# Kernel tuning notes

Measured on AMD Instinct MI355X. Metric: run time of the kernel, lower is better.

The kernel has to match this reference:

```python
import jax, jax.numpy as jnp
import numpy as np
import math

Q_DIM = 1024
K_DIM = 1024
ATT_DIM = 1024
POS_DIM = 64
B, NQ, NK = 4, 2048, 2048
EPS = 1e-5


def _ln(x, g, b):
    m = jnp.mean(x, axis=-1, keepdims=True)
    v = jnp.var(x, axis=-1, keepdims=True)
    return (x - m) * jax.lax.rsqrt(v + EPS) * g + b


def _sinpos(n, dim):
    # SinPos: exp = 2*arange(dim//2)/dim; pos = p * 10000**-exp; cat(pos, pos+pi/2); sin
    e = 2.0 * jnp.arange(dim // 2, dtype=jnp.float32) / dim      # [dim/2]
    p = jnp.arange(n, dtype=jnp.float32)[:, None]                # [n,1]
    ph = p * jnp.power(10000.0, -e)[None, :]                     # [n,dim/2]
    return jnp.sin(jnp.concatenate([ph, ph + math.pi / 2], axis=1))  # [n,dim]


def setup_inputs() -> dict:
    key = jax.random.key(0)
    ks = jax.random.split(key, 8)
    s = 0.02
    return {
        "q": jax.random.normal(ks[0], (B, NQ, Q_DIM), jnp.float32),
        "k": jax.random.normal(ks[1], (B, NK, K_DIM), jnp.float32),
        "Wq": jax.random.normal(ks[2], (Q_DIM, ATT_DIM), jnp.float32) * s,
        "bq": jnp.zeros((ATT_DIM,), jnp.float32),
        "Wk": jax.random.normal(ks[3], (K_DIM, ATT_DIM), jnp.float32) * s,
        "bk": jnp.zeros((ATT_DIM,), jnp.float32),
        "Wv": jax.random.normal(ks[4], (K_DIM, ATT_DIM), jnp.float32) * s,
        "bv": jnp.zeros((ATT_DIM,), jnp.float32),
        "gq": jnp.ones((ATT_DIM,), jnp.float32), "betaq": jnp.zeros((ATT_DIM,), jnp.float32),
        "gk": jnp.ones((ATT_DIM,), jnp.float32), "betak": jnp.zeros((ATT_DIM,), jnp.float32),
        "gv": jnp.ones((ATT_DIM,), jnp.float32), "betav": jnp.zeros((ATT_DIM,), jnp.float32),
        "Wp": jax.random.normal(ks[5], (POS_DIM, POS_DIM), jnp.float32) * s,
        "bp": jnp.zeros((POS_DIM,), jnp.float32),
    }


def reference(q, k, Wq, bq, Wk, bk, Wv, bv, gq, betaq, gk, betak, gv, betav, Wp, bp):
    qn = _ln(q @ Wq + bq, gq, betaq)          # [B,NQ,D]
    vn = _ln(k @ Wv + bv, gv, betav)          # [B,NK,D]
    kn = _ln(k @ Wk + bk, gk, betak)          # [B,NK,D]
    pos = _sinpos(NK, POS_DIM)                # [NK,P]

    # attention 1: Q=qn, K=kn, V=pos
    s1 = jnp.einsum('bnd,bjd->bnj', qn, kn) * (1.0 / math.sqrt(ATT_DIM))
    a1 = jax.nn.softmax(s1, axis=-1)          # [B,NQ,NK]
    x = jnp.einsum('bnj,jp->bnp', a1, pos)    # [B,NQ,P]

    # pos_net (Linear)
    x = x @ Wp + bp                           # [B,NQ,P]

    # attention 2: Q=x, K=pos, V=vn
    s2 = jnp.einsum('bnp,jp->bnj', x, pos) * (1.0 / math.sqrt(POS_DIM))
    a2 = jax.nn.softmax(s2, axis=-1)          # [B,NQ,NK]
    out = jnp.einsum('bnj,bjd->bnd', a2, vn)  # [B,NQ,D]

    att = jnp.stack([a1, a2], axis=1)         # [B,2,NQ,NK] == torch.cat over head dim
    return out, att
```

## Files before the change

### kernel.cpp

```cpp
#include <hip/hip_runtime.h>
#include <math.h>
#include <stdint.h>


typedef _Float16 f16;
typedef _Float16 f16x4 __attribute__((ext_vector_type(4)));
typedef _Float16 f16x8 __attribute__((ext_vector_type(8)));
typedef float f32x4 __attribute__((ext_vector_type(4)));

static constexpr int CB  = 4;
static constexpr int CNQ = 2048;
static constexpr int CNK = 2048;
static constexpr int CD  = 1024;
static constexpr int CP  = 64;

static __device__ __forceinline__ void async16(const f16* gp, f16* lp) {
  __builtin_amdgcn_global_load_lds(
      (const __attribute__((address_space(1))) void*)(uintptr_t)gp,
      (__attribute__((address_space(3))) void*)(uint32_t)(uintptr_t)lp,
      16, 0, 0);
}

__global__ __launch_bounds__(256) void prep_kernel(
    const float* __restrict__ q, const float* __restrict__ k,
    const float* __restrict__ Wq, const float* __restrict__ Wk,
    const float* __restrict__ Wv,
    f16* __restrict__ q16, f16* __restrict__ k16,
    f16* __restrict__ WqT, f16* __restrict__ WkvT,
    f16* __restrict__ posb, f16* __restrict__ posTb) {
  const int b = blockIdx.x;
  if (b < 512) {
    int tid = b * 256 + threadIdx.x;
    int p = tid >> 11;
    int j = tid & (CNK - 1);
    int i = p & 31;
    float ph = (float)j * powf(10000.0f, -(float)i * (1.0f / 32.0f));
    float v = (p < 32) ? sinf(ph) : cosf(ph);
    posb[j * CP + p]   = (f16)v;
    posTb[p * CNK + j] = (f16)v;
  } else if (b < 512 + 16384) {
    const int NF4 = CB * CNQ * CD / 4;
    int tid = (b - 512) * 256 + threadIdx.x;
    const float* src = (tid < NF4) ? q : k;
    f16* dst = (tid < NF4) ? q16 : k16;
    int i = (tid < NF4) ? tid : tid - NF4;
    float4 v = reinterpret_cast<const float4*>(src)[i];
    f16x4 o = {(f16)v.x, (f16)v.y, (f16)v.z, (f16)v.w};
    reinterpret_cast<f16x4*>(dst)[i] = o;
  } else {
    __shared__ float t[64][65];
    const int idx = b - 16896;
    const int z = idx >> 8;
    const int rem = idx & 255;
    const float* W = (z == 0) ? Wq : (z == 1) ? Wk : Wv;
    f16* WT = (z == 0) ? WqT : (z == 1) ? WkvT : WkvT + 1024 * 1024;
    int k0 = (rem & 15) * 64, n0 = (rem >> 4) * 64;
    int tx = threadIdx.x & 63, ty = threadIdx.x >> 6;
#pragma unroll
    for (int i = 0; i < 16; i++)
      t[ty + 4 * i][tx] = W[(size_t)(k0 + ty + 4 * i) * CD + n0 + tx];
    __syncthreads();
#pragma unroll
    for (int i = 0; i < 16; i++)
      WT[(size_t)(n0 + 4 * i + ty) * CD + k0 + tx] = (f16)t[tx][ty + 4 * i];
  }
}

template <int BM, int BN>
__device__ __forceinline__ void gemm_core2(
    const f16* __restrict__ Ab, const f16* __restrict__ Bb,
    int lda, int ldb, int K, int m0, int n0, f16* sm,
    f32x4 (&acc)[BM / 32][4]) {
  constexpr int FM = BM / 32;
  constexpr int TI = (BM + BN) / 64;
  constexpr int bufsz = (BM + BN) * 64;
  const int tid = threadIdx.x;
  const int lane = tid & 63, wid = tid >> 6;
  const int wr = wid >> 2, wc = wid & 3;
  const int lrow = lane & 15, kg = lane >> 4;

  auto stage = [&](int i, int kt, int buf) {
    const int s = i * 512 + tid;
    const int row = s >> 3;
    const int cb = (s & 7) << 4;
    const int scb = cb ^ ((row & 7) << 4);
    const f16* src = (i < BM / 64)
        ? Ab + (size_t)(m0 + row) * lda + kt * 64 + (scb >> 1)
        : Bb + (size_t)(n0 + row - BM) * ldb + kt * 64 + (scb >> 1);
    async16(src, &sm[buf * bufsz + s * 8]);
  };

  const int NTk = K >> 6;
#pragma unroll
  for (int i = 0; i < TI; i++) stage(i, 0, 0);

  for (int t = 0; t < NTk; ++t) {
    const int cur = t & 1;
    if (t + 1 < NTk) {
#pragma unroll
      for (int i = 0; i < TI; i++) stage(i, t + 1, cur ^ 1);
      if constexpr (TI == 8) asm volatile("s_waitcnt vmcnt(8)" ::: "memory");
      else                   asm volatile("s_waitcnt vmcnt(6)" ::: "memory");
    } else {
      asm volatile("s_waitcnt vmcnt(0)" ::: "memory");
    }
    __builtin_amdgcn_s_barrier();

    const f16* smA = sm + cur * bufsz;
    const f16* smB = smA + BM * 64;
    __builtin_amdgcn_s_setprio(1);
#pragma unroll
    for (int kk = 0; kk < 2; ++kk) {
      const int Cb = kk * 64 + kg * 16;
      f16x8 af[FM], bf[4];
#pragma unroll
      for (int m = 0; m < FM; ++m) {
        const int ar = wr * (BM / 2) + m * 16 + lrow;
        af[m] = *reinterpret_cast<const f16x8*>(
            &smA[ar * 64 + ((Cb ^ ((ar & 7) << 4)) >> 1)]);
      }
#pragma unroll
      for (int n = 0; n < 4; ++n) {
        const int br = wc * 64 + n * 16 + lrow;
        bf[n] = *reinterpret_cast<const f16x8*>(
            &smB[br * 64 + ((Cb ^ ((br & 7) << 4)) >> 1)]);
      }
#pragma unroll
      for (int m = 0; m < FM; ++m)
#pragma unroll
        for (int n = 0; n < 4; ++n)
          acc[m][n] = __builtin_amdgcn_mfma_f32_16x16x32_f16(af[m], bf[n], acc[m][n], 0, 0, 0);
    }
    __builtin_amdgcn_s_setprio(0);
    __builtin_amdgcn_s_barrier();
  }
}

template <int BM, int BN>
__device__ __forceinline__ void epi_f16(
    f32x4 (&acc)[BM / 32][4], f16* sm, f16* Cp, int ldc, int m0, int n0) {
  const int tid = threadIdx.x, lane = tid & 63, wid = tid >> 6;
  const int wr = wid >> 2, wc = wid & 3;
  const int rbase = wr * (BM / 2) + (lane >> 4) * 4;
  const int cbase = wc * 64 + (lane & 15);
  __syncthreads();
#pragma unroll
  for (int mg = 0; mg < BM / 32; mg++)
#pragma unroll
    for (int n = 0; n < 4; n++)
#pragma unroll
      for (int r = 0; r < 4; r++)
        sm[(rbase + mg * 16 + r) * BN + cbase + n * 16] = (f16)acc[mg][n][r];
  __syncthreads();
  constexpr int CH = BM * BN / (512 * 8);
#pragma unroll
  for (int c = 0; c < CH; c++) {
    const int idx = c * 512 + tid;
    const int row = idx / (BN / 8);
    const int cole = (idx % (BN / 8)) * 8;
    f16x8 v = *reinterpret_cast<const f16x8*>(&sm[row * BN + cole]);
    *reinterpret_cast<f16x8*>(Cp + (size_t)(m0 + row) * ldc + n0 + cole) = v;
  }
}

template <int BM, int BN>
__device__ __forceinline__ void epi_exp(
    f32x4 (&acc)[BM / 32][4], f16* sm, float* psum, f16* Cp, int ldc,
    int m0, int n0, float scale, float* PSrow) {
  constexpr int SL = BN / 8;
  const int tid = threadIdx.x, lane = tid & 63, wid = tid >> 6;
  const int wr = wid >> 2, wc = wid & 3;
  const int rbase = wr * (BM / 2) + (lane >> 4) * 4;
  const int cbase = wc * 64 + (lane & 15);
  __syncthreads();
#pragma unroll
  for (int mg = 0; mg < BM / 32; mg++)
#pragma unroll
    for (int n = 0; n < 4; n++)
#pragma unroll
      for (int r = 0; r < 4; r++)
        sm[(rbase + mg * 16 + r) * BN + cbase + n * 16] =
            (f16)__expf(acc[mg][n][r] * scale);
  __syncthreads();
  constexpr int CH = BM * BN / (512 * 8);
#pragma unroll
  for (int c = 0; c < CH; c++) {
    const int idx = c * 512 + tid;
    const int row = idx / SL;
    const int cole = (idx % SL) * 8;
    f16x8 v = *reinterpret_cast<const f16x8*>(&sm[row * BN + cole]);
    *reinterpret_cast<f16x8*>(Cp + (size_t)(m0 + row) * ldc + n0 + cole) = v;
    float p = 0.f;
#pragma unroll
    for (int j = 0; j < 8; j++) p += (float)v[j];
#pragma unroll
    for (int o = 1; o < SL; o <<= 1) p += __shfl_xor(p, o);
    if ((lane & (SL - 1)) == 0) psum[row] = p;
  }
  __syncthreads();
  if (tid < BM) PSrow[tid] = psum[tid];
}

template <int BM, int BN>
__device__ __forceinline__ void epi_f32(
    f32x4 (&acc)[BM / 32][4], f16* smh, float* Cp, int ldc, int m0, int n0) {
  float* st = (float*)smh;
  const int tid = threadIdx.x, lane = tid & 63, wid = tid >> 6;
  const int wr = wid >> 2, wc = wid & 3;
  const int cbase = wc * 64 + (lane & 15);
#pragma unroll
  for (int half = 0; half < 2; half++) {
    __syncthreads();
    if (wr == half) {
#pragma unroll
      for (int mg = 0; mg < BM / 32; mg++)
#pragma unroll
        for (int r = 0; r < 4; r++) {
          const int rloc = (lane >> 4) * 4 + mg * 16 + r;
#pragma unroll
          for (int n = 0; n < 4; n++)
            st[rloc * BN + cbase + n * 16] = acc[mg][n][r];
        }
    }
    __syncthreads();
    constexpr int CH = (BM / 2) * BN / (512 * 4);
#pragma unroll
    for (int c = 0; c < CH; c++) {
      const int idx = c * 512 + tid;
      const int row = idx / (BN / 4);
      const int cole = (idx % (BN / 4)) * 4;
      f32x4 v = *reinterpret_cast<const f32x4*>(&st[row * BN + cole]);
      *reinterpret_cast<f32x4*>(
          Cp + (size_t)(m0 + half * (BM / 2) + row) * ldc + n0 + cole) = v;
    }
  }
}

__global__ __launch_bounds__(512) void gemmIn_kernel(
    const f16* __restrict__ q16, const f16* __restrict__ WqT, f16* __restrict__ tmpq,
    const f16* __restrict__ k16, const f16* __restrict__ WkvT, f16* __restrict__ tmp2) {
  __shared__ __attribute__((aligned(16))) f16 sm[2 * (128 + 256) * 64];
  const int b = blockIdx.x;
  const int swz = (b & 7) * 96 + (b >> 3);
  const f16 *A, *B;
  f16* C;
  int ldc, m0, n0;
  if (swz < 256) {
    const int bx = swz & 63, by = swz >> 6;
    A = q16; B = WqT; C = tmpq; ldc = 1024; m0 = bx * 128; n0 = by * 256;
  } else {
    const int idx = swz - 256;
    const int bx = idx & 63, by = idx >> 6;
    A = k16; B = WkvT; C = tmp2; ldc = 2048; m0 = bx * 128; n0 = by * 256;
  }
  f32x4 acc[4][4] = {};
  gemm_core2<128, 256>(A, B, 1024, 1024, 1024, m0, n0, sm, acc);
  epi_f16<128, 256>(acc, sm, C, ldc, m0, n0);
}

__global__ __launch_bounds__(512) void gemmS1_kernel(
    const f16* __restrict__ qn, const f16* __restrict__ kn,
    f16* __restrict__ e1, float* __restrict__ PS) {
  __shared__ __attribute__((aligned(16))) f16 sm[2 * (256 + 256) * 64];
  __shared__ float psum[256];
  const int b = blockIdx.x;
  const int swz = (b & 7) * 32 + (b >> 3);
  const int bz = swz >> 6;
  const int rem = swz & 63;
  const int bx = rem & 7, by = rem >> 3;
  const int m0 = bx * 256, n0 = by * 256;
  const f16* Ab = qn + (size_t)bz * 2048 * 1024;
  const f16* Bb = kn + (size_t)bz * 2048 * 2048;
  f16* Cp = e1 + (size_t)bz * 2048 * 2048;
  f32x4 acc[8][4] = {};
  gemm_core2<256, 256>(Ab, Bb, 1024, 2048, 1024, m0, n0, sm, acc);
  epi_exp<256, 256>(acc, sm, psum, Cp, 2048, m0, n0, 0.03125f,
                    PS + (size_t)by * (CB * CNQ) + bz * 2048 + m0);
}

__global__ __launch_bounds__(512) void gemmOut_kernel(
    const f16* __restrict__ e2, const f16* __restrict__ vnT, float* __restrict__ out) {
  __shared__ __attribute__((aligned(16))) f16 sm[2 * (128 + 256) * 64];
  const int b = blockIdx.x;
  const int swz = (b & 7) * 32 + (b >> 3);
  const int bz = swz >> 6;
  const int rem = swz & 63;
  const int bx = rem & 15, by = rem >> 4;
  const int m0 = bx * 128, n0 = by * 256;
  const f16* Ab = e2 + (size_t)bz * 2048 * 2048;
  const f16* Bb = vnT + (size_t)bz * 1024 * 2048;
  float* Cp = out + (size_t)bz * 2048 * 1024;
  f32x4 acc[4][4] = {};
  gemm_core2<128, 256>(Ab, Bb, 2048, 2048, 2048, m0, n0, sm, acc);
  epi_f32<128, 256>(acc, sm, Cp, 1024, m0, n0);
}

__global__ __launch_bounds__(256) void ln3_kernel(
    f16* __restrict__ tmpq, f16* __restrict__ tmp2, float* __restrict__ vstat,
    const float* __restrict__ bq, const float* __restrict__ gq, const float* __restrict__ beq,
    const float* __restrict__ bk, const float* __restrict__ gk, const float* __restrict__ bek,
    const float* __restrict__ bv) {
  __shared__ float rs_[4], rq_[4];
  const int z = blockIdx.y;
  f16* rp;
  const float *bias, *g, *beta;
  if (z == 0)      { rp = tmpq + (size_t)blockIdx.x * 1024;        bias = bq; g = gq; beta = beq; }
  else if (z == 1) { rp = tmp2 + (size_t)blockIdx.x * 2048;        bias = bk; g = gk; beta = bek; }
  else             { rp = tmp2 + (size_t)blockIdx.x * 2048 + 1024; bias = bv; g = nullptr; beta = nullptr; }
  const int t = threadIdx.x;
  f16x4 v = *reinterpret_cast<const f16x4*>(rp + t * 4);
  float y[4], s = 0.f, q = 0.f;
#pragma unroll
  for (int j = 0; j < 4; j++) {
    y[j] = (float)v[j] + bias[t * 4 + j];
    s += y[j]; q += y[j] * y[j];
  }
#pragma unroll
  for (int o = 32; o; o >>= 1) { s += __shfl_xor(s, o); q += __shfl_xor(q, o); }
  if ((t & 63) == 0) { rs_[t >> 6] = s; rq_[t >> 6] = q; }
  __syncthreads();
  s = rs_[0] + rs_[1] + rs_[2] + rs_[3];
  q = rq_[0] + rq_[1] + rq_[2] + rq_[3];
  const float mean = s * (1.0f / CD);
  const float rstd = rsqrtf(q * (1.0f / CD) - mean * mean + 1e-5f);
  if (z == 2) {
    if (t == 0) { vstat[blockIdx.x] = mean; vstat[CB * CNK + blockIdx.x] = rstd; }
    return;
  }
  f16x4 o;
#pragma unroll
  for (int j = 0; j < 4; j++) {
    int c = t * 4 + j;
    o[j] = (f16)((y[j] - mean) * rstd * g[c] + beta[c]);
  }
  *reinterpret_cast<f16x4*>(rp + t * 4) = o;
}

__global__ __launch_bounds__(256) void transposeLN_kernel(
    const f16* __restrict__ tmp2, f16* __restrict__ vnT,
    const float* __restrict__ vstat, const float* __restrict__ bv,
    const float* __restrict__ gv, const float* __restrict__ bev) {
  __shared__ f16 t[64][65];
  __shared__ float ms[64], rs[64];
  int n0 = blockIdx.x * 64, d0 = blockIdx.y * 64;
  size_t ibase = (size_t)blockIdx.z * CNK * 2048;
  size_t obase = (size_t)blockIdx.z * CNK * CD;
  int tx = threadIdx.x & 63, ty = threadIdx.x >> 6;
  const int tokbase = blockIdx.z * CNK + n0;
  if (threadIdx.x < 64) {
    ms[threadIdx.x] = vstat[tokbase + threadIdx.x];
    rs[threadIdx.x] = vstat[CB * CNK + tokbase + threadIdx.x];
  }
#pragma unroll
  for (int i = 0; i < 16; i++)
    t[ty + 4 * i][tx] = tmp2[ibase + (size_t)(n0 + ty + 4 * i) * 2048 + 1024 + d0 + tx];
  __syncthreads();
#pragma unroll
  for (int i = 0; i < 16; i++) {
    const int dim = d0 + 4 * i + ty;
    const float yv = (float)t[tx][ty + 4 * i] + bv[dim];
    vnT[obase + (size_t)dim * CNK + n0 + tx] =
        (f16)((yv - ms[tx]) * rs[tx] * gv[dim] + bev[dim]);
  }
}

__global__ __launch_bounds__(512) void xgemm_kernel(
    const f16* __restrict__ e1, const f16* __restrict__ posTb,
    const float* __restrict__ PS, float* __restrict__ xw, float* __restrict__ att) {
  __shared__ __attribute__((aligned(16))) f16 sm[2 * 128 * 64];
  __shared__ float invs[64];
  const int tid = threadIdx.x, lane = tid & 63, wid = tid >> 6;
  const int wr = wid >> 1, wc = wid & 1;
  const int lrow = lane & 15, kg = lane >> 4;
  const int m0 = blockIdx.x * 64;
  const int kbase = blockIdx.z * 1024;

  if (tid < 64) {
    float s = 0.f;
#pragma unroll
    for (int j = 0; j < 8; j++) s += PS[j * (CB * CNQ) + m0 + tid];
    invs[tid] = 1.0f / s;
  }

  auto stage = [&](int i, int kt, int buf) {
    const int s = i * 512 + tid;
    const int row = s >> 3;
    const int cb = (s & 7) << 4;
    const int scb = cb ^ ((row & 7) << 4);
    const f16* src = (row < 64)
        ? e1 + (size_t)(m0 + row) * CNK + kbase + kt * 64 + (scb >> 1)
        : posTb + (size_t)(row - 64) * CNK + kbase + kt * 64 + (scb >> 1);
    async16(src, &sm[buf * (128 * 64) + s * 8]);
  };

  const int bb = m0 >> 11, nloc = m0 & (CNQ - 1);
  float* attb = att + ((size_t)(bb << 1) * CNQ + nloc) * CNK + kbase;
  const int arow = tid >> 3, acb = tid & 7;

  f32x4 acc[2] = {};
  const int NTk = 16;
#pragma unroll
  for (int i = 0; i < 2; i++) stage(i, 0, 0);

  for (int t = 0; t < NTk; ++t) {
    const int cur = t & 1;
    if (t + 1 < NTk) {
#pragma unroll
      for (int i = 0; i < 2; i++) stage(i, t + 1, cur ^ 1);
      asm volatile("s_waitcnt vmcnt(2)" ::: "memory");
    } else {
      asm volatile("s_waitcnt vmcnt(0)" ::: "memory");
    }
    __builtin_amdgcn_s_barrier();
    const f16* smA = sm + cur * (128 * 64);
    const f16* smB = smA + 64 * 64;
#pragma unroll
    for (int kk = 0; kk < 2; ++kk) {
      const int Cb = kk * 64 + kg * 16;
      const int ar = wr * 16 + lrow;
      f16x8 af = *reinterpret_cast<const f16x8*>(
          &smA[ar * 64 + ((Cb ^ ((ar & 7) << 4)) >> 1)]);
#pragma unroll
      for (int n = 0; n < 2; ++n) {
        const int br = wc * 32 + n * 16 + lrow;
        f16x8 bf = *reinterpret_cast<const f16x8*>(
            &smB[br * 64 + ((Cb ^ ((br & 7) << 4)) >> 1)]);
        acc[n] = __builtin_amdgcn_mfma_f32_16x16x32_f16(af, bf, acc[n], 0, 0, 0);
      }
    }
    {
      const float iv = invs[arow];
      f16x8 v = *reinterpret_cast<const f16x8*>(
          &smA[arow * 64 + ((acb ^ (arow & 7)) << 3)]);
      f32x4 w0 = {(float)v[0] * iv, (float)v[1] * iv, (float)v[2] * iv, (float)v[3] * iv};
      f32x4 w1 = {(float)v[4] * iv, (float)v[5] * iv, (float)v[6] * iv, (float)v[7] * iv};
      float* ap = attb + (size_t)arow * CNK + t * 64 + acb * 8;
      *reinterpret_cast<f32x4*>(ap)     = w0;
      *reinterpret_cast<f32x4*>(ap + 4) = w1;
    }
    __builtin_amdgcn_s_barrier();
  }

  float* Cp = xw + (size_t)blockIdx.z * (CB * CNQ) * CP;
  const int crow = m0 + wr * 16 + (lane >> 4) * 4;
  const int ccol = wc * 32 + (lane & 15);
#pragma unroll
  for (int n = 0; n < 2; n++)
#pragma unroll
    for (int r = 0; r < 4; r++)
      Cp[(size_t)(crow + r) * CP + ccol + n * 16] = acc[n][r];
}

__global__ __launch_bounds__(512) void attn2_kernel(
    const float* __restrict__ xw, const float* __restrict__ Wp,
    const float* __restrict__ bp, const f16* __restrict__ posb,
    const float* __restrict__ PS, f16* __restrict__ e2,
    float* __restrict__ att) {
  constexpr int ELD = 2056;
  __shared__ __attribute__((aligned(16))) f16 shm[16 * ELD + 16 * 64];
  __shared__ float rsum8[8][16];
  __shared__ float invs[16];
  f16* e2lds = shm;
  f16* xpb = shm + 16 * ELD;
  float* xs = (float*)shm;
  float* Wps = (float*)shm + 16 * 64;
  const int tid = threadIdx.x, l = tid & 63, w = tid >> 6;
  const int r0 = blockIdx.x * 16;
  if (tid < 16) {
    float s = 0.f;
#pragma unroll
    for (int j = 0; j < 8; j++) s += PS[j * (CB * CNQ) + r0 + tid];
    invs[tid] = 1.0f / s;
  }
  __syncthreads();
  if (w < 2) {
#pragma unroll
    for (int i = 0; i < 8; i++) {
      const int row = w * 8 + i;
      const size_t gi = (size_t)(r0 + row) * CP + l;
      xs[row * 64 + l] = (xw[gi] + xw[(size_t)(CB * CNQ) * CP + gi]) * invs[row];
    }
#pragma unroll
    for (int i = w; i < 64; i += 2) Wps[i * 64 + l] = Wp[i * 64 + l];
  }
  const float bpl = bp[l];
  __syncthreads();
  if (w < 2) {
#pragma unroll 2
    for (int i = 0; i < 8; i++) {
      const int row = w * 8 + i;
      float a = bpl;
#pragma unroll 8
      for (int p = 0; p < 64; p++) a = fmaf(xs[row * 64 + p], Wps[p * 64 + l], a);
      xpb[row * 64 + l] = (f16)a;
    }
  }
  __syncthreads();
  const f16x8 af0 = *reinterpret_cast<const f16x8*>(&xpb[(l & 15) * 64 + (l >> 4) * 8]);
  const f16x8 af1 = *reinterpret_cast<const f16x8*>(&xpb[(l & 15) * 64 + 32 + (l >> 4) * 8]);
  float rs[4] = {0.f, 0.f, 0.f, 0.f};
  for (int jt = w * 4; jt < w * 4 + 4; jt++) {
#pragma unroll
    for (int q4 = 0; q4 < 4; q4++) {
      const int j = jt * 64 + q4 * 16 + (l & 15);
      const f16* pp = posb + (size_t)j * CP + (l >> 4) * 8;
      f16x8 b0 = *reinterpret_cast<const f16x8*>(pp);
      f16x8 b1 = *reinterpret_cast<const f16x8*>(pp + 32);
      f32x4 c = {};
      c = __builtin_amdgcn_mfma_f32_16x16x32_f16(af0, b0, c, 0, 0, 0);
      c = __builtin_amdgcn_mfma_f32_16x16x32_f16(af1, b1, c, 0, 0, 0);
#pragma unroll
      for (int r = 0; r < 4; r++) {
        float ev = __expf(c[r] * 0.125f);
        rs[r] += ev;
        e2lds[((l >> 4) * 4 + r) * ELD + j] = (f16)ev;
      }
    }
  }
#pragma unroll
  for (int r = 0; r < 4; r++) {
#pragma unroll
    for (int o = 1; o < 16; o <<= 1) rs[r] += __shfl_xor(rs[r], o);
    if ((l & 15) == 0) rsum8[w][(l >> 4) * 4 + r] = rs[r];
  }
  __syncthreads();
  const int b = r0 >> 11, nloc = r0 & (CNQ - 1);
  float* attb = att + ((size_t)((b << 1) + 1) * CNQ + nloc) * CNK;
  f16* e2b = e2 + (size_t)r0 * CNK;
  for (int it = 0; it < 4; it++) {
    const int row = it * 4 + (tid >> 7);
    const int col = (tid & 127) * 16;
    float s = 0.f;
#pragma unroll
    for (int h = 0; h < 8; h++) s += rsum8[h][row];
    const float iv = 1.0f / s;
    const f16x8 a0 = *reinterpret_cast<const f16x8*>(&e2lds[row * ELD + col]);
    const f16x8 a1 = *reinterpret_cast<const f16x8*>(&e2lds[row * ELD + col + 8]);
    f32x4 w0 = {(float)a0[0] * iv, (float)a0[1] * iv, (float)a0[2] * iv, (float)a0[3] * iv};
    f32x4 w1 = {(float)a0[4] * iv, (float)a0[5] * iv, (float)a0[6] * iv, (float)a0[7] * iv};
    f32x4 w2 = {(float)a1[0] * iv, (float)a1[1] * iv, (float)a1[2] * iv, (float)a1[3] * iv};
    f32x4 w3 = {(float)a1[4] * iv, (float)a1[5] * iv, (float)a1[6] * iv, (float)a1[7] * iv};
    float* ap = attb + (size_t)row * CNK + col;
    *reinterpret_cast<f32x4*>(ap)      = w0;
    *reinterpret_cast<f32x4*>(ap + 4)  = w1;
    *reinterpret_cast<f32x4*>(ap + 8)  = w2;
    *reinterpret_cast<f32x4*>(ap + 12) = w3;
    f16x8 h0 = {(f16)w0[0], (f16)w0[1], (f16)w0[2], (f16)w0[3],
                (f16)w1[0], (f16)w1[1], (f16)w1[2], (f16)w1[3]};
    f16x8 h1 = {(f16)w2[0], (f16)w2[1], (f16)w2[2], (f16)w2[3],
                (f16)w3[0], (f16)w3[1], (f16)w3[2], (f16)w3[3]};
    f16* ep = e2b + (size_t)row * CNK + col;
    *reinterpret_cast<f16x8*>(ep)     = h0;
    *reinterpret_cast<f16x8*>(ep + 8) = h1;
  }
}

extern "C" void kernel_launch(void* const* d_in, const int* in_sizes, int n_in,
                              void* d_out, int out_size, void* d_ws, size_t ws_size,
                              hipStream_t stream) {
  (void)in_sizes; (void)n_in; (void)out_size; (void)ws_size;
  const float* q    = (const float*)d_in[0];
  const float* k    = (const float*)d_in[1];
  const float* Wq   = (const float*)d_in[2];
  const float* bq   = (const float*)d_in[3];
  const float* Wk   = (const float*)d_in[4];
  const float* bk   = (const float*)d_in[5];
  const float* Wv   = (const float*)d_in[6];
  const float* bv   = (const float*)d_in[7];
  const float* gq   = (const float*)d_in[8];
  const float* betaq= (const float*)d_in[9];
  const float* gk   = (const float*)d_in[10];
  const float* betak= (const float*)d_in[11];
  const float* gv   = (const float*)d_in[12];
  const float* betav= (const float*)d_in[13];
  const float* Wp   = (const float*)d_in[14];
  const float* bp   = (const float*)d_in[15];

  float* out = (float*)d_out;
  float* att = out + (size_t)CB * CNQ * CD;
  char* ws = (char*)d_ws;
  const size_t MB = 1ull << 20;

  f16* q16   = (f16*)(ws);
  f16* k16   = (f16*)(ws + 16 * MB);
  f16* e1    = (f16*)(ws);
  f16* e2    = (f16*)(ws);
  f16* WqT   = (f16*)(ws + 32 * MB);
  f16* WkvT  = (f16*)(ws + 34 * MB);
  f16* posb  = (f16*)(ws + 38 * MB);
  f16* posTb = (f16*)(ws + 38 * MB + 256 * 1024);
  float* xw  = (float*)(ws + 38 * MB + 512 * 1024);
  float* PS  = (float*)(ws + 42 * MB + 512 * 1024);
  float* vstat = (float*)(ws + 42 * MB + 768 * 1024);
  f16* tmpq  = (f16*)(ws + 43 * MB);
  f16* tmp2  = (f16*)(ws + 59 * MB);
  f16* vnT   = (f16*)(ws + 91 * MB);
  f16* qn = tmpq;
  f16* kn = tmp2;

  prep_kernel<<<512 + 16384 + 768, 256, 0, stream>>>(
      q, k, Wq, Wk, Wv, q16, k16, WqT, WkvT, posb, posTb);

  gemmIn_kernel<<<768, 512, 0, stream>>>(q16, WqT, tmpq, k16, WkvT, tmp2);
  ln3_kernel<<<dim3(CB * CNQ, 3), 256, 0, stream>>>(
      tmpq, tmp2, vstat, bq, gq, betaq, bk, gk, betak, bv);
  transposeLN_kernel<<<dim3(CNK / 64, CD / 64, CB), 256, 0, stream>>>(
      tmp2, vnT, vstat, bv, gv, betav);

  gemmS1_kernel<<<256, 512, 0, stream>>>(qn, kn, e1, PS);

  xgemm_kernel<<<dim3(CB * CNQ / 64, 1, 2), 512, 0, stream>>>(e1, posTb, PS, xw, att);
  attn2_kernel<<<CB * CNQ / 16, 512, 0, stream>>>(xw, Wp, bp, posb, PS, e2, att);

  gemmOut_kernel<<<256, 512, 0, stream>>>(e2, vnT, out);
}
```

Baseline: 281.2 us.

## Fuse x-GEMM and attention-1 probability write into attn2 kernel

Removes the separate xgemm kernel and computes x = a1 @ pos inside attn2. Each block now reads its 16 rows of e1 directly from global memory, writes the normalized a1 probabilities, and runs MFMAs against posTb split across 8 waves. Partial sums are reduced through LDS, which drops the xw round-trip and one kernel launch. In exchange, every block re-reads the full posTb (256KB) from global or L2 without LDS staging, and each block has a smaller M tile, so reuse of posTb is lower.

```diff
diff --git a/kernel.cpp b/kernel.cpp
--- a/kernel.cpp
+++ b/kernel.cpp
@@ -364,106 +364,20 @@
   }
 }
 
-__global__ __launch_bounds__(512) void xgemm_kernel(
+__global__ __launch_bounds__(512) void attn2_kernel(
     const f16* __restrict__ e1, const f16* __restrict__ posTb,
-    const float* __restrict__ PS, float* __restrict__ xw, float* __restrict__ att) {
-  __shared__ __attribute__((aligned(16))) f16 sm[2 * 128 * 64];
-  __shared__ float invs[64];
-  const int tid = threadIdx.x, lane = tid & 63, wid = tid >> 6;
-  const int wr = wid >> 1, wc = wid & 1;
-  const int lrow = lane & 15, kg = lane >> 4;
-  const int m0 = blockIdx.x * 64;
-  const int kbase = blockIdx.z * 1024;
-
-  if (tid < 64) {
-    float s = 0.f;
-#pragma unroll
-    for (int j = 0; j < 8; j++) s += PS[j * (CB * CNQ) + m0 + tid];
-    invs[tid] = 1.0f / s;
-  }
-
-  auto stage = [&](int i, int kt, int buf) {
-    const int s = i * 512 + tid;
-    const int row = s >> 3;
-    const int cb = (s & 7) << 4;
-    const int scb = cb ^ ((row & 7) << 4);
-    const f16* src = (row < 64)
-        ? e1 + (size_t)(m0 + row) * CNK + kbase + kt * 64 + (scb >> 1)
-        : posTb + (size_t)(row - 64) * CNK + kbase + kt * 64 + (scb >> 1);
-    async16(src, &sm[buf * (128 * 64) + s * 8]);
-  };
-
-  const int bb = m0 >> 11, nloc = m0 & (CNQ - 1);
-  float* attb = att + ((size_t)(bb << 1) * CNQ + nloc) * CNK + kbase;
-  const int arow = tid >> 3, acb = tid & 7;
-
-  f32x4 acc[2] = {};
-  const int NTk = 16;
-#pragma unroll
-  for (int i = 0; i < 2; i++) stage(i, 0, 0);
-
-  for (int t = 0; t < NTk; ++t) {
-    const int cur = t & 1;
-    if (t + 1 < NTk) {
-#pragma unroll
-      for (int i = 0; i < 2; i++) stage(i, t + 1, cur ^ 1);
-      asm volatile("s_waitcnt vmcnt(2)" ::: "memory");
-    } else {
-      asm volatile("s_waitcnt vmcnt(0)" ::: "memory");
-    }
-    __builtin_amdgcn_s_barrier();
-    const f16* smA = sm + cur * (128 * 64);
-    const f16* smB = smA + 64 * 64;
-#pragma unroll
-    for (int kk = 0; kk < 2; ++kk) {
-      const int Cb = kk * 64 + kg * 16;
-      const int ar = wr * 16 + lrow;
-      f16x8 af = *reinterpret_cast<const f16x8*>(
-          &smA[ar * 64 + ((Cb ^ ((ar & 7) << 4)) >> 1)]);
-#pragma unroll
-      for (int n = 0; n < 2; ++n) {
-        const int br = wc * 32 + n * 16 + lrow;
-        f16x8 bf = *reinterpret_cast<const f16x8*>(
-            &smB[br * 64 + ((Cb ^ ((br & 7) << 4)) >> 1)]);
-        acc[n] = __builtin_amdgcn_mfma_f32_16x16x32_f16(af, bf, acc[n], 0, 0, 0);
-      }
-    }
-    {
-      const float iv = invs[arow];
-      f16x8 v = *reinterpret_cast<const f16x8*>(
-          &smA[arow * 64 + ((acb ^ (arow & 7)) << 3)]);
-      f32x4 w0 = {(float)v[0] * iv, (float)v[1] * iv, (float)v[2] * iv, (float)v[3] * iv};
-      f32x4 w1 = {(float)v[4] * iv, (float)v[5] * iv, (float)v[6] * iv, (float)v[7] * iv};
-      float* ap = attb + (size_t)arow * CNK + t * 64 + acb * 8;
-      *reinterpret_cast<f32x4*>(ap)     = w0;
-      *reinterpret_cast<f32x4*>(ap + 4) = w1;
-    }
-    __builtin_amdgcn_s_barrier();
-  }
-
-  float* Cp = xw + (size_t)blockIdx.z * (CB * CNQ) * CP;
-  const int crow = m0 + wr * 16 + (lane >> 4) * 4;
-  const int ccol = wc * 32 + (lane & 15);
-#pragma unroll
-  for (int n = 0; n < 2; n++)
-#pragma unroll
-    for (int r = 0; r < 4; r++)
-      Cp[(size_t)(crow + r) * CP + ccol + n * 16] = acc[n][r];
-}
-
-__global__ __launch_bounds__(512) void attn2_kernel(
-    const float* __restrict__ xw, const float* __restrict__ Wp,
-    const float* __restrict__ bp, const f16* __restrict__ posb,
-    const float* __restrict__ PS, f16* __restrict__ e2,
-    float* __restrict__ att) {
+    const float* __restrict__ Wp, const float* __restrict__ bp,
+    const f16* __restrict__ posb, const float* __restrict__ PS,
+    f16* __restrict__ e2, float* __restrict__ att) {
   constexpr int ELD = 2056;
   __shared__ __attribute__((aligned(16))) f16 shm[16 * ELD + 16 * 64];
   __shared__ float rsum8[8][16];
   __shared__ float invs[16];
   f16* e2lds = shm;
   f16* xpb = shm + 16 * ELD;
-  float* xs = (float*)shm;
-  float* Wps = (float*)shm + 16 * 64;
+  float* part = (float*)shm;
+  float* xs   = (float*)shm + 8 * 1024;
+  float* Wps  = (float*)shm + 9 * 1024;
   const int tid = threadIdx.x, l = tid & 63, w = tid >> 6;
   const int r0 = blockIdx.x * 16;
   if (tid < 16) {
@@ -473,18 +387,50 @@
     invs[tid] = 1.0f / s;
   }
   __syncthreads();
-  if (w < 2) {
-#pragma unroll
-    for (int i = 0; i < 8; i++) {
-      const int row = w * 8 + i;
-      const size_t gi = (size_t)(r0 + row) * CP + l;
-      xs[row * 64 + l] = (xw[gi] + xw[(size_t)(CB * CNQ) * CP + gi]) * invs[row];
-    }
-#pragma unroll
-    for (int i = w; i < 64; i += 2) Wps[i * 64 + l] = Wp[i * 64 + l];
-  }
+
+  const int row16 = l & 15, kg8 = (l >> 4) * 8;
+  const int bb = r0 >> 11, nloc = r0 & (CNQ - 1);
+  float* att0b = att + ((size_t)(bb << 1) * CNQ + nloc) * CNK;
+  const float ivr = invs[row16];
+  f32x4 xacc[4] = {};
+#pragma unroll
+  for (int i = 0; i < 8; i++) {
+    const int kcol = w * 256 + i * 32 + kg8;
+    f16x8 af = *reinterpret_cast<const f16x8*>(
+        &e1[(size_t)(r0 + row16) * CNK + kcol]);
+    f32x4 w0 = {(float)af[0] * ivr, (float)af[1] * ivr,
+                (float)af[2] * ivr, (float)af[3] * ivr};
+    f32x4 w1 = {(float)af[4] * ivr, (float)af[5] * ivr,
+                (float)af[6] * ivr, (float)af[7] * ivr};
+    float* ap = att0b + (size_t)row16 * CNK + kcol;
+    *reinterpret_cast<f32x4*>(ap)     = w0;
+    *reinterpret_cast<f32x4*>(ap + 4) = w1;
+#pragma unroll
+    for (int nf = 0; nf < 4; nf++) {
+      f16x8 bf = *reinterpret_cast<const f16x8*>(
+          &posTb[(size_t)(nf * 16 + row16) * CNK + kcol]);
+      xacc[nf] = __builtin_amdgcn_mfma_f32_16x16x32_f16(af, bf, xacc[nf], 0, 0, 0);
+    }
+  }
+#pragma unroll
+  for (int nf = 0; nf < 4; nf++)
+#pragma unroll
+    for (int r = 0; r < 4; r++)
+      part[w * 1024 + ((l >> 4) * 4 + r) * 64 + nf * 16 + (l & 15)] = xacc[nf][r];
+  __syncthreads();
+
+#pragma unroll
+  for (int idx = tid; idx < 1024; idx += 512) {
+    float s = 0.f;
+#pragma unroll
+    for (int h = 0; h < 8; h++) s += part[h * 1024 + idx];
+    xs[idx] = s * invs[idx >> 6];
+  }
+#pragma unroll
+  for (int idx = tid; idx < 4096; idx += 512) Wps[idx] = Wp[idx];
   const float bpl = bp[l];
   __syncthreads();
+
   if (w < 2) {
 #pragma unroll 2
     for (int i = 0; i < 8; i++) {
@@ -496,6 +442,7 @@
     }
   }
   __syncthreads();
+
   const f16x8 af0 = *reinterpret_cast<const f16x8*>(&xpb[(l & 15) * 64 + (l >> 4) * 8]);
   const f16x8 af1 = *reinterpret_cast<const f16x8*>(&xpb[(l & 15) * 64 + 32 + (l >> 4) * 8]);
   float rs[4] = {0.f, 0.f, 0.f, 0.f};
@@ -524,8 +471,8 @@
     if ((l & 15) == 0) rsum8[w][(l >> 4) * 4 + r] = rs[r];
   }
   __syncthreads();
-  const int b = r0 >> 11, nloc = r0 & (CNQ - 1);
-  float* attb = att + ((size_t)((b << 1) + 1) * CNQ + nloc) * CNK;
+
+  float* att1b = att + ((size_t)((bb << 1) + 1) * CNQ + nloc) * CNK;
   f16* e2b = e2 + (size_t)r0 * CNK;
   for (int it = 0; it < 4; it++) {
     const int row = it * 4 + (tid >> 7);
@@ -540,7 +487,7 @@
     f32x4 w1 = {(float)a0[4] * iv, (float)a0[5] * iv, (float)a0[6] * iv, (float)a0[7] * iv};
     f32x4 w2 = {(float)a1[0] * iv, (float)a1[1] * iv, (float)a1[2] * iv, (float)a1[3] * iv};
     f32x4 w3 = {(float)a1[4] * iv, (float)a1[5] * iv, (float)a1[6] * iv, (float)a1[7] * iv};
-    float* ap = attb + (size_t)row * CNK + col;
+    float* ap = att1b + (size_t)row * CNK + col;
     *reinterpret_cast<f32x4*>(ap)      = w0;
     *reinterpret_cast<f32x4*>(ap + 4)  = w1;
     *reinterpret_cast<f32x4*>(ap + 8)  = w2;
@@ -589,7 +536,6 @@
   f16* WkvT  = (f16*)(ws + 34 * MB);
   f16* posb  = (f16*)(ws + 38 * MB);
   f16* posTb = (f16*)(ws + 38 * MB + 256 * 1024);
-  float* xw  = (float*)(ws + 38 * MB + 512 * 1024);
   float* PS  = (float*)(ws + 42 * MB + 512 * 1024);
   float* vstat = (float*)(ws + 42 * MB + 768 * 1024);
   f16* tmpq  = (f16*)(ws + 43 * MB);
@@ -609,8 +555,8 @@
 
   gemmS1_kernel<<<256, 512, 0, stream>>>(qn, kn, e1, PS);
 
-  xgemm_kernel<<<dim3(CB * CNQ / 64, 1, 2), 512, 0, stream>>>(e1, posTb, PS, xw, att);
-  attn2_kernel<<<CB * CNQ / 16, 512, 0, stream>>>(xw, Wp, bp, posb, PS, e2, att);
+  attn2_kernel<<<CB * CNQ / 16, 512, 0, stream>>>(
+      e1, posTb, Wp, bp, posb, PS, e2, att);
 
   gemmOut_kernel<<<256, 512, 0, stream>>>(e2, vnT, out);
 }
```

Result: no change. 284.0 us (+1.0%).
